# Kernel optimization log

Hardware: AMD Instinct MI355X
Metric: run time of the kernel (lower is better)

Reference implementation:

```python
import jax, jax.numpy as jnp
import numpy as np

B, S, T, D, H, HD = 1, 2048, 256, 3072, 24, 128
FF = 4 * D
EPS_LN = 1e-6
EPS_RMS = 1e-6


def _layernorm(x):
    m = jnp.mean(x, axis=-1, keepdims=True)
    v = jnp.mean(jnp.square(x - m), axis=-1, keepdims=True)
    return (x - m) * jax.lax.rsqrt(v + EPS_LN)


def _rmsnorm(x, w):
    return x * jax.lax.rsqrt(jnp.mean(jnp.square(x), axis=-1, keepdims=True) + EPS_RMS) * w


def _rope_interleaved(x, cos, sin):
    # x: [B,S,H,HD], cos/sin: [S,HD//2]; non-neox (interleaved) style
    x1 = x[..., 0::2]
    x2 = x[..., 1::2]
    c = cos[None, :, None, :]
    s = sin[None, :, None, :]
    o1 = x1 * c - x2 * s
    o2 = x2 * c + x1 * s
    return jnp.stack([o1, o2], axis=-1).reshape(x.shape)


def setup_inputs() -> dict:
    key = jax.random.key(0)
    ks = jax.random.split(key, 12)

    def n(k, shape, scale):
        return jax.random.normal(k, shape, dtype=jnp.float32) * scale

    # real RoPE tables
    pos = np.arange(S, dtype=np.float64)
    inv_freq = 1.0 / (10000.0 ** (np.arange(0, HD, 2, dtype=np.float64) / HD))
    ang = np.outer(pos, inv_freq)  # [S, HD//2]

    return {
        "img": n(ks[0], (B, S, D), 1.0),
        "vec": n(ks[1], (B, D), 1.0),
        "cos": jnp.asarray(np.cos(ang), jnp.float32),
        "sin": jnp.asarray(np.sin(ang), jnp.float32),
        "k_txt": n(ks[2], (B, T, H, HD), 1.0),
        "v_txt": n(ks[3], (B, T, H, HD), 1.0),
        "mod_w": n(ks[4], (D, 6 * D), 0.02),
        "mod_b": jnp.zeros((6 * D,), jnp.float32),
        "qkv_w": n(ks[5], (D, 3 * D), 0.02),
        "qkv_b": jnp.zeros((3 * D,), jnp.float32),
        "qn_w": jnp.ones((HD,), jnp.float32),
        "kn_w": jnp.ones((HD,), jnp.float32),
        "proj_w": n(ks[6], (D, D), 0.02),
        "proj_b": jnp.zeros((D,), jnp.float32),
        "mlp_w1": n(ks[7], (D, FF), 0.02),
        "mlp_b1": jnp.zeros((FF,), jnp.float32),
        "mlp_w2": n(ks[8], (FF, D), 0.02),
        "mlp_b2": jnp.zeros((D,), jnp.float32),
    }


def reference(img, vec, cos, sin, k_txt, v_txt, mod_w, mod_b, qkv_w, qkv_b,
              qn_w, kn_w, proj_w, proj_b, mlp_w1, mlp_b1, mlp_w2, mlp_b2):
    # modulation: silu(vec) -> linear -> 6 chunks, each [B,1,D]
    mod = jax.nn.silu(vec) @ mod_w + mod_b
    (a_shift, a_scale, a_gate, m_shift, m_scale, m_gate) = [
        m[:, None, :] for m in jnp.split(mod, 6, axis=-1)
    ]

    # LayerNorm (no affine) + scale/shift modulate
    x = _layernorm(img) * (1.0 + a_scale) + a_shift

    qkv = (x @ qkv_w + qkv_b).reshape(B, S, 3, H, HD)
    q, k, v = qkv[:, :, 0], qkv[:, :, 1], qkv[:, :, 2]
    q = _rmsnorm(q, qn_w)
    k = _rmsnorm(k, kn_w)
    q = _rope_interleaved(q, cos, sin)
    k = _rope_interleaved(k, cos, sin)

    # concat text KV cache (no RoPE on text tokens)
    k_all = jnp.concatenate([k, k_txt], axis=1)  # [B,S+T,H,HD]
    v_all = jnp.concatenate([v, v_txt], axis=1)

    scale = 1.0 / jnp.sqrt(jnp.asarray(HD, jnp.float32))
    scores = jnp.einsum('bqhd,bkhd->bhqk', q, k_all) * scale
    probs = jax.nn.softmax(scores, axis=-1)
    attn = jnp.einsum('bhqk,bkhd->bqhd', probs, v_all).reshape(B, S, D)

    attn_out = attn @ proj_w + proj_b

    # ScaleResidualLayerNormScaleShift
    residual = img + a_gate * attn_out
    mlp_in = _layernorm(residual) * (1.0 + m_scale) + m_shift

    mlp_out = jax.nn.gelu(mlp_in @ mlp_w1 + mlp_b1, approximate=True) @ mlp_w2 + mlp_b2
    return residual + m_gate * mlp_out
```

## Files before the change

kernel.cpp:

```cpp
#include <hip/hip_runtime.h>

typedef short short8 __attribute__((ext_vector_type(8)));
typedef float f32x4 __attribute__((ext_vector_type(4)));

#define DEV static __device__ __forceinline__

DEV unsigned short f2bf(float f) {
  union { float f; unsigned u; } v; v.f = f;
  unsigned u = v.u;
  unsigned r = u + 0x7fffu + ((u >> 16) & 1u);
  return (unsigned short)(r >> 16);
}
DEV float bf2f(unsigned short b) {
  union { unsigned u; float f; } v; v.u = ((unsigned)b) << 16;
  return v.f;
}
DEV void load_lds16(const void* g, void* l) {
  __builtin_amdgcn_global_load_lds(
      (const __attribute__((address_space(1))) unsigned int*)g,
      (__attribute__((address_space(3))) unsigned int*)l, 16, 0, 0);
}
DEV int swz(int L) { return L ^ ((L >> 3) & 0x30); }

__global__ __launch_bounds__(256) void zero_mod(const float* __restrict__ b, float* __restrict__ out) {
  int j = blockIdx.x * 256 + threadIdx.x;
  out[j] = b[j];
}

__global__ __launch_bounds__(256) void mod_gemv(const float* __restrict__ vec,
                                                const float* __restrict__ W,
                                                float* __restrict__ out) {
  __shared__ float sv[192];
  int tid = threadIdx.x;
  int kb = blockIdx.y * 192;
  if (tid < 192) {
    float x = vec[kb + tid];
    sv[tid] = x / (1.f + __expf(-x));
  }
  __syncthreads();
  int j = blockIdx.x * 256 + tid;
  float a0 = 0, a1 = 0, a2 = 0, a3 = 0;
  for (int i = 0; i < 192; i += 4) {
    a0 += sv[i + 0] * W[(size_t)(kb + i + 0) * 18432 + j];
    a1 += sv[i + 1] * W[(size_t)(kb + i + 1) * 18432 + j];
    a2 += sv[i + 2] * W[(size_t)(kb + i + 2) * 18432 + j];
    a3 += sv[i + 3] * W[(size_t)(kb + i + 3) * 18432 + j];
  }
  atomicAdd(&out[j], a0 + a1 + a2 + a3);
}

__global__ __launch_bounds__(256) void ln_kernel(const float* __restrict__ in,
                                                 const float* __restrict__ mod,
                                                 int shift_off, int scale_off,
                                                 unsigned short* __restrict__ out) {
  int rowb = blockIdx.x;
  const float* x = in + (size_t)rowb * 3072;
  int tid = threadIdx.x;
  float s = 0.f, ss = 0.f;
  float4 v[3];
#pragma unroll
  for (int r = 0; r < 3; r++) {
    v[r] = *(const float4*)&x[r * 1024 + tid * 4];
    s += v[r].x + v[r].y + v[r].z + v[r].w;
    ss += v[r].x * v[r].x + v[r].y * v[r].y + v[r].z * v[r].z + v[r].w * v[r].w;
  }
#pragma unroll
  for (int m = 32; m; m >>= 1) { s += __shfl_xor(s, m); ss += __shfl_xor(ss, m); }
  __shared__ float red[8];
  int w = tid >> 6, lane = tid & 63;
  if (lane == 0) { red[w] = s; red[4 + w] = ss; }
  __syncthreads();
  s = red[0] + red[1] + red[2] + red[3];
  ss = red[4] + red[5] + red[6] + red[7];
  float mean = s * (1.f / 3072.f);
  float var = ss * (1.f / 3072.f) - mean * mean;
  float rstd = rsqrtf(var + 1e-6f);
#pragma unroll
  for (int r = 0; r < 3; r++) {
    int c = r * 1024 + tid * 4;
    float xv[4] = {v[r].x, v[r].y, v[r].z, v[r].w};
#pragma unroll
    for (int i = 0; i < 4; i++) {
      float o = (xv[i] - mean) * rstd * (1.f + mod[scale_off + c + i]) + mod[shift_off + c + i];
      out[(size_t)rowb * 3072 + c + i] = f2bf(o);
    }
  }
}

__global__ __launch_bounds__(256) void transpose_k(const float* __restrict__ src,
                                                   unsigned short* __restrict__ dst,
                                                   int K, int N) {
  __shared__ float t[64][65];
  int n0 = blockIdx.x * 64, k0 = blockIdx.y * 64;
  int tid = threadIdx.x;
#pragma unroll
  for (int i = 0; i < 16; i++) {
    int lin = i * 256 + tid;
    int r = lin >> 6, c = lin & 63;
    t[r][c] = src[(size_t)(k0 + r) * N + n0 + c];
  }
  __syncthreads();
#pragma unroll
  for (int i = 0; i < 16; i++) {
    int lin = i * 256 + tid;
    int rn = lin >> 6, cn = lin & 63;
    dst[(size_t)(n0 + rn) * K + k0 + cn] = f2bf(t[cn][rn]);
  }
}

template <int EPI>
__global__ __launch_bounds__(512, 2) void gemm8(const unsigned short* __restrict__ A,
                                                const unsigned short* __restrict__ Bt,
                                                const float* __restrict__ bias,
                                                unsigned short* __restrict__ outb,
                                                int N, int ldk, int klen) {
  __shared__ unsigned short As[4][8192];
  __shared__ unsigned short Bs[4][8192];
  const int tid = threadIdx.x, lane = tid & 63, w = tid >> 6;
  const int wr = w >> 2, wc = w & 3;
  const int lr = lane & 15, lk = lane >> 4;

  const int bm = blockIdx.y * 256, bn = blockIdx.x * 256;
  const int kbase = blockIdx.z * klen;
  const int NT = klen >> 5;

  const int D0 = tid * 16;
  const int D1 = 8192 + tid * 16;
  const int L0 = swz(D0), L1 = swz(D1);
  const unsigned short* sA0 = A + (size_t)(bm + (L0 >> 6)) * ldk + kbase + ((L0 & 63) >> 1);
  const unsigned short* sA1 = A + (size_t)(bm + (L1 >> 6)) * ldk + kbase + ((L1 & 63) >> 1);
  const unsigned short* sB0 = Bt + (size_t)(bn + (L0 >> 6)) * ldk + kbase + ((L0 & 63) >> 1);
  const unsigned short* sB1 = Bt + (size_t)(bn + (L1 >> 6)) * ldk + kbase + ((L1 & 63) >> 1);

  int aoff[8], boff[4];
#pragma unroll
  for (int mi = 0; mi < 8; mi++)
    aoff[mi] = swz(((wr * 128 + mi * 16 + lr) << 6) | (lk << 4));
#pragma unroll
  for (int ni = 0; ni < 4; ni++)
    boff[ni] = swz(((wc * 64 + ni * 16 + lr) << 6) | (lk << 4));

  f32x4 acc[8][4];
#pragma unroll
  for (int i = 0; i < 8; i++)
#pragma unroll
    for (int j = 0; j < 4; j++) acc[i][j] = (f32x4){0.f, 0.f, 0.f, 0.f};

#pragma unroll
  for (int j = 0; j < 3; j++) {
    load_lds16(sA0 + j * 32, (char*)As + j * 16384 + D0);
    load_lds16(sA1 + j * 32, (char*)As + j * 16384 + D1);
    load_lds16(sB0 + j * 32, (char*)Bs + j * 16384 + D0);
    load_lds16(sB1 + j * 32, (char*)Bs + j * 16384 + D1);
  }
  asm volatile("s_waitcnt vmcnt(8)" ::: "memory");
  __builtin_amdgcn_sched_barrier(0);
  __builtin_amdgcn_s_barrier();

  for (int t = 0; t < NT; ++t) {
    const int rt = t & 3;
    char* Ab = (char*)As + rt * 16384;
    char* Bb = (char*)Bs + rt * 16384;
    const int ss = (t + 3) & 3;
    const int sk = (t + 3) * 32;
    const bool stg = (t + 3) < NT;

    short8 af[8], bf[4];
#pragma unroll
    for (int mi = 0; mi < 8; mi++) af[mi] = *(const short8*)(Ab + aoff[mi]);
#pragma unroll
    for (int ni = 0; ni < 4; ni++) bf[ni] = *(const short8*)(Bb + boff[ni]);
    if (stg) {
      load_lds16(sA0 + sk, (char*)As + ss * 16384 + D0);
      load_lds16(sA1 + sk, (char*)As + ss * 16384 + D1);
      load_lds16(sB0 + sk, (char*)Bs + ss * 16384 + D0);
      load_lds16(sB1 + sk, (char*)Bs + ss * 16384 + D1);
    }
    __builtin_amdgcn_s_setprio(1);
#pragma unroll
    for (int mi = 0; mi < 8; mi++)
#pragma unroll
      for (int ni = 0; ni < 4; ni++)
        acc[mi][ni] = __builtin_amdgcn_mfma_f32_16x16x32_bf16(af[mi], bf[ni], acc[mi][ni], 0, 0, 0);
    __builtin_amdgcn_s_setprio(0);
    if (t < NT - 3) {
      asm volatile("s_waitcnt vmcnt(8)" ::: "memory");
    } else if (t == NT - 3) {
      asm volatile("s_waitcnt vmcnt(4)" ::: "memory");
    } else if (t == NT - 2) {
      asm volatile("s_waitcnt vmcnt(0)" ::: "memory");
    }
    __builtin_amdgcn_sched_barrier(0);
    __builtin_amdgcn_s_barrier();
  }

  const size_t zoff = (size_t)blockIdx.z * ((size_t)2048 * N);
#pragma unroll
  for (int mi = 0; mi < 8; mi++) {
#pragma unroll
    for (int ni = 0; ni < 4; ni++) {
      int row0 = bm + wr * 128 + mi * 16 + lk * 4;
      int col = bn + wc * 64 + ni * 16 + lr;
#pragma unroll
      for (int r = 0; r < 4; r++) {
        float vv = acc[mi][ni][r];
        if (EPI == 0) {
          outb[(size_t)(row0 + r) * N + col] = f2bf(vv + bias[col]);
        } else if (EPI == 2) {
          float x = vv + bias[col];
          float y = 0.7978845608028654f * (x + 0.044715f * x * x * x);
          float th = 1.f - 2.f / (__expf(2.f * y) + 1.f);
          outb[(size_t)(row0 + r) * N + col] = f2bf(0.5f * x * (1.f + th));
        } else {
          outb[zoff + (size_t)(row0 + r) * N + col] = f2bf(vv);
        }
      }
    }
  }
}

__global__ __launch_bounds__(256) void sk_epi(const unsigned short* __restrict__ pb,
                                              const float* __restrict__ bias,
                                              const float* __restrict__ addsrc,
                                              const float* __restrict__ gate,
                                              float* __restrict__ out) {
  const int N = 3072;
  const size_t MN = (size_t)2048 * 3072;
  int row = blockIdx.y;
  int col = blockIdx.x * 1024 + threadIdx.x * 4;
  size_t idx = (size_t)row * N + col;
  const unsigned short* p0 = pb + idx;
  const unsigned short* p1 = pb + MN + idx;
  float4 a = *(const float4*)(addsrc + idx);
  float4 b = *(const float4*)(bias + col);
  float4 g = *(const float4*)(gate + col);
  float4 o;
  o.x = a.x + g.x * (bf2f(p0[0]) + bf2f(p1[0]) + b.x);
  o.y = a.y + g.y * (bf2f(p0[1]) + bf2f(p1[1]) + b.y);
  o.z = a.z + g.z * (bf2f(p0[2]) + bf2f(p1[2]) + b.z);
  o.w = a.w + g.w * (bf2f(p0[3]) + bf2f(p1[3]) + b.w);
  *(float4*)(out + idx) = o;
}

__global__ __launch_bounds__(64) void qkv_post(const unsigned short* __restrict__ qkv,
                                               const float* __restrict__ k_txt,
                                               const float* __restrict__ v_txt,
                                               const float* __restrict__ cosb,
                                               const float* __restrict__ sinb,
                                               const float* __restrict__ qn,
                                               const float* __restrict__ kn,
                                               unsigned short* __restrict__ qb,
                                               unsigned short* __restrict__ kb,
                                               unsigned short* __restrict__ vb) {
  int s = blockIdx.x, h = blockIdx.y;
  int lane = threadIdx.x;
  int d0 = lane * 2;
  if (s < 2048) {
    const unsigned short* rowp = qkv + (size_t)s * 9216;
    float c = cosb[s * 64 + lane], sn = sinb[s * 64 + lane];
    const float ascale = 0.08838834764831845f;
    {
      float a = bf2f(rowp[h * 128 + d0]), b = bf2f(rowp[h * 128 + d0 + 1]);
      float sq = a * a + b * b;
#pragma unroll
      for (int m = 32; m; m >>= 1) sq += __shfl_xor(sq, m);
      float rr = rsqrtf(sq * (1.f / 128.f) + 1e-6f);
      float x1 = a * rr * qn[d0], x2 = b * rr * qn[d0 + 1];
      float o1 = (x1 * c - x2 * sn) * ascale;
      float o2 = (x2 * c + x1 * sn) * ascale;
      size_t off = ((size_t)h * 2048 + s) * 128 + d0;
      qb[off] = f2bf(o1); qb[off + 1] = f2bf(o2);
    }
    {
      float a = bf2f(rowp[3072 + h * 128 + d0]), b = bf2f(rowp[3072 + h * 128 + d0 + 1]);
      float sq = a * a + b * b;
#pragma unroll
      for (int m = 32; m; m >>= 1) sq += __shfl_xor(sq, m);
      float rr = rsqrtf(sq * (1.f / 128.f) + 1e-6f);
      float x1 = a * rr * kn[d0], x2 = b * rr * kn[d0 + 1];
      float o1 = x1 * c - x2 * sn;
      float o2 = x2 * c + x1 * sn;
      size_t off = ((size_t)h * 2304 + s) * 128 + d0;
      kb[off] = f2bf(o1); kb[off + 1] = f2bf(o2);
    }
    {
      float a = bf2f(rowp[6144 + h * 128 + d0]), b = bf2f(rowp[6144 + h * 128 + d0 + 1]);
      size_t off = ((size_t)h * 2304 + s) * 128 + d0;
      vb[off] = f2bf(a); vb[off + 1] = f2bf(b);
    }
  } else {
    int t = s - 2048;
    size_t src = ((size_t)t * 24 + h) * 128 + d0;
    size_t off = ((size_t)h * 2304 + s) * 128 + d0;
    kb[off] = f2bf(k_txt[src]); kb[off + 1] = f2bf(k_txt[src + 1]);
    vb[off] = f2bf(v_txt[src]); vb[off + 1] = f2bf(v_txt[src + 1]);
  }
}

__global__ __launch_bounds__(256) void attn_k(const unsigned short* __restrict__ qb,
                                              const unsigned short* __restrict__ kb,
                                              const unsigned short* __restrict__ vb,
                                              unsigned short* __restrict__ out) {
  __shared__ unsigned short Ks[64 * 128];
  __shared__ unsigned short Vs[128 * 64];
  __shared__ unsigned short Ps[4][16 * 64];
  int h = blockIdx.y, q0 = blockIdx.x * 64;
  int tid = threadIdx.x, lane = tid & 63, w = tid >> 6;
  int lr = lane & 15, lk = lane >> 4;

  const unsigned short* kh = kb + (size_t)h * 2304 * 128;
  const unsigned short* vh = vb + (size_t)h * 2304 * 128;

  short8 qf[4];
#pragma unroll
  for (int kf = 0; kf < 4; kf++)
    qf[kf] = *(const short8*)&qb[((size_t)h * 2048 + q0 + w * 16 + lr) * 128 + kf * 32 + lk * 8];

  float mrow[4] = {-1e30f, -1e30f, -1e30f, -1e30f};
  float lsum[4] = {0.f, 0.f, 0.f, 0.f};
  f32x4 oacc[8];
#pragma unroll
  for (int i = 0; i < 8; i++) oacc[i] = (f32x4){0.f, 0.f, 0.f, 0.f};

  for (int kt = 0; kt < 36; kt++) {
    int kv0 = kt * 64;
    __syncthreads();
#pragma unroll
    for (int i = 0; i < 4; i++) {
      int o = (w * 4 + i) * 1024 + lane * 16;
      int n = o >> 8;
      int sl = (o >> 4) & 15;
      int c = sl ^ (n & 15);
      load_lds16((const char*)(kh + (size_t)(kv0 + n) * 128) + c * 16, (char*)Ks + o);
    }
#pragma unroll
    for (int r = 0; r < 4; r++) {
      int e = r * 2048 + tid * 8;
      int kv = e >> 7, dd0 = e & 127;
      short8 val = *(const short8*)&vh[(size_t)(kv0 + kv) * 128 + dd0];
#pragma unroll
      for (int j = 0; j < 8; j++) {
        int d = dd0 + j;
        int fs = (d & 7) ^ ((d >> 3) & 7);
        Vs[d * 64 + (((kv >> 3) ^ fs) << 3) + (kv & 7)] = (unsigned short)val[j];
      }
    }
    __syncthreads();

    f32x4 sa[4];
#pragma unroll
    for (int ni = 0; ni < 4; ni++) sa[ni] = (f32x4){0.f, 0.f, 0.f, 0.f};
#pragma unroll
    for (int kf = 0; kf < 4; kf++) {
#pragma unroll
      for (int ni = 0; ni < 4; ni++) {
        int n = ni * 16 + lr;
        int slot = (kf * 4 + lk) ^ (n & 15);
        short8 bfr = *(const short8*)&Ks[n * 128 + slot * 8];
        sa[ni] = __builtin_amdgcn_mfma_f32_16x16x32_bf16(qf[kf], bfr, sa[ni], 0, 0, 0);
      }
    }

    float pv[4][4];
#pragma unroll
    for (int r = 0; r < 4; r++) {
      float mx = fmaxf(fmaxf(sa[0][r], sa[1][r]), fmaxf(sa[2][r], sa[3][r]));
#pragma unroll
      for (int m = 8; m; m >>= 1) mx = fmaxf(mx, __shfl_xor(mx, m));
      float mnew = fmaxf(mrow[r], mx);
      float su = 0.f;
#pragma unroll
      for (int ni = 0; ni < 4; ni++) {
        float p = __expf(sa[ni][r] - mnew);
        pv[ni][r] = p;
        su += p;
      }
#pragma unroll
      for (int m = 8; m; m >>= 1) su += __shfl_xor(su, m);
      float alpha = __expf(mrow[r] - mnew);
      lsum[r] = lsum[r] * alpha + su;
      mrow[r] = mnew;
#pragma unroll
      for (int df = 0; df < 8; df++) oacc[df][r] *= alpha;
    }
#pragma unroll
    for (int ni = 0; ni < 4; ni++)
#pragma unroll
      for (int r = 0; r < 4; r++) {
        int row = lk * 4 + r, col = ni * 16 + lr;
        Ps[w][row * 64 + ((((col >> 3) ^ (row & 7))) << 3) + (col & 7)] = f2bf(pv[ni][r]);
      }

#pragma unroll
    for (int kf2 = 0; kf2 < 2; kf2++) {
      short8 pa = *(const short8*)&Ps[w][lr * 64 + (((kf2 * 4 + lk) ^ (lr & 7)) << 3)];
#pragma unroll
      for (int df = 0; df < 8; df++) {
        int d = df * 16 + lr;
        int fs = (d & 7) ^ ((d >> 3) & 7);
        short8 bv = *(const short8*)&Vs[d * 64 + (((kf2 * 4 + lk) ^ fs) << 3)];
        oacc[df] = __builtin_amdgcn_mfma_f32_16x16x32_bf16(pa, bv, oacc[df], 0, 0, 0);
      }
    }
  }

#pragma unroll
  for (int r = 0; r < 4; r++) {
    float inv = 1.f / lsum[r];
    int row = q0 + w * 16 + lk * 4 + r;
#pragma unroll
    for (int df = 0; df < 8; df++)
      out[(size_t)row * 3072 + h * 128 + df * 16 + lr] = f2bf(oacc[df][r] * inv);
  }
}

extern "C" void kernel_launch(void* const* d_in, const int* in_sizes, int n_in,
                              void* d_out, int out_size, void* d_ws, size_t ws_size,
                              hipStream_t stream) {
  const float* img = (const float*)d_in[0];
  const float* vec = (const float*)d_in[1];
  const float* cosb = (const float*)d_in[2];
  const float* sinb = (const float*)d_in[3];
  const float* k_txt = (const float*)d_in[4];
  const float* v_txt = (const float*)d_in[5];
  const float* mod_w = (const float*)d_in[6];
  const float* mod_b = (const float*)d_in[7];
  const float* qkv_w = (const float*)d_in[8];
  const float* qkv_b = (const float*)d_in[9];
  const float* qn_w = (const float*)d_in[10];
  const float* kn_w = (const float*)d_in[11];
  const float* proj_w = (const float*)d_in[12];
  const float* proj_b = (const float*)d_in[13];
  const float* mlp_w1 = (const float*)d_in[14];
  const float* mlp_b1 = (const float*)d_in[15];
  const float* mlp_w2 = (const float*)d_in[16];
  const float* mlp_b2 = (const float*)d_in[17];
  float* outp = (float*)d_out;

  char* ws = (char*)d_ws;
  unsigned short* qkvb = (unsigned short*)(ws + 0);
  unsigned short* qbuf = (unsigned short*)(ws + 37748736);
  unsigned short* kbuf = (unsigned short*)(ws + 50331648);
  unsigned short* vbuf = (unsigned short*)(ws + 64487424);
  unsigned short* attnb = (unsigned short*)(ws + 78643200);
  float* resid = (float*)(ws + 91226112);
  unsigned short* xln = (unsigned short*)(ws + 116391936);
  float* modv = (float*)(ws + 128974848);
  unsigned short* wt = (unsigned short*)(ws + 129048576);
  unsigned short* hbuf = (unsigned short*)(ws + 0);
  unsigned short* pbuf = (unsigned short*)(ws + 50331648);

  zero_mod<<<72, 256, 0, stream>>>(mod_b, modv);
  mod_gemv<<<dim3(72, 16), 256, 0, stream>>>(vec, mod_w, modv);

  ln_kernel<<<2048, 256, 0, stream>>>(img, modv, 0, 3072, xln);

  transpose_k<<<dim3(144, 48), 256, 0, stream>>>(qkv_w, wt, 3072, 9216);
  gemm8<0><<<dim3(36, 8, 1), 512, 0, stream>>>(xln, wt, qkv_b, qkvb, 9216, 3072, 3072);

  qkv_post<<<dim3(2304, 24), 64, 0, stream>>>(qkvb, k_txt, v_txt, cosb, sinb,
                                              qn_w, kn_w, qbuf, kbuf, vbuf);

  attn_k<<<dim3(32, 24), 256, 0, stream>>>(qbuf, kbuf, vbuf, attnb);

  transpose_k<<<dim3(48, 48), 256, 0, stream>>>(proj_w, wt, 3072, 3072);
  gemm8<3><<<dim3(12, 8, 2), 512, 0, stream>>>(attnb, wt, nullptr, pbuf, 3072, 3072, 1536);
  sk_epi<<<dim3(3, 2048), 256, 0, stream>>>(pbuf, proj_b, img, modv + 2 * 3072, resid);

  ln_kernel<<<2048, 256, 0, stream>>>(resid, modv, 3 * 3072, 4 * 3072, xln);

  transpose_k<<<dim3(192, 48), 256, 0, stream>>>(mlp_w1, wt, 3072, 12288);
  gemm8<2><<<dim3(48, 8, 1), 512, 0, stream>>>(xln, wt, mlp_b1, hbuf, 12288, 3072, 3072);

  transpose_k<<<dim3(48, 192), 256, 0, stream>>>(mlp_w2, wt, 12288, 3072);
  gemm8<3><<<dim3(12, 8, 2), 512, 0, stream>>>(hbuf, wt, nullptr, pbuf, 3072, 12288, 6144);
  sk_epi<<<dim3(3, 2048), 256, 0, stream>>>(pbuf, mlp_b2, resid, modv + 5 * 3072, outp);
}
```

Measured before the change: 989.2 us.

## Pre-transpose V and double-buffer K/V tiles in larger attention blocks

```diff
diff --git a/kernel.cpp b/kernel.cpp
--- a/kernel.cpp
+++ b/kernel.cpp
@@ -106,6 +106,26 @@
     int rn = lin >> 6, cn = lin & 63;
     dst[(size_t)(n0 + rn) * K + k0 + cn] = f2bf(t[cn][rn]);
   }
+}
+
+__global__ __launch_bounds__(256) void vt_k(const unsigned short* __restrict__ qkvb,
+                                            const float* __restrict__ v_txt,
+                                            unsigned short* __restrict__ vt) {
+  int h = blockIdx.y;
+  int c8 = blockIdx.x * 2 + (threadIdx.x >> 7);
+  int d = threadIdx.x & 127;
+  int kvb = c8 * 8;
+  short8 o;
+  if (kvb < 2048) {
+#pragma unroll
+    for (int j = 0; j < 8; j++)
+      o[j] = (short)qkvb[(size_t)(kvb + j) * 9216 + 6144 + h * 128 + d];
+  } else {
+#pragma unroll
+    for (int j = 0; j < 8; j++)
+      o[j] = (short)f2bf(v_txt[((size_t)(kvb + j - 2048) * 24 + h) * 128 + d]);
+  }
+  *(short8*)&vt[((size_t)h * 128 + d) * 2304 + kvb] = o;
 }
 
 template <int EPI>
@@ -244,14 +264,12 @@
 
 __global__ __launch_bounds__(64) void qkv_post(const unsigned short* __restrict__ qkv,
                                                const float* __restrict__ k_txt,
-                                               const float* __restrict__ v_txt,
                                                const float* __restrict__ cosb,
                                                const float* __restrict__ sinb,
                                                const float* __restrict__ qn,
                                                const float* __restrict__ kn,
                                                unsigned short* __restrict__ qb,
-                                               unsigned short* __restrict__ kb,
-                                               unsigned short* __restrict__ vb) {
+                                               unsigned short* __restrict__ kb) {
   int s = blockIdx.x, h = blockIdx.y;
   int lane = threadIdx.x;
   int d0 = lane * 2;
@@ -283,134 +301,149 @@
       size_t off = ((size_t)h * 2304 + s) * 128 + d0;
       kb[off] = f2bf(o1); kb[off + 1] = f2bf(o2);
     }
-    {
-      float a = bf2f(rowp[6144 + h * 128 + d0]), b = bf2f(rowp[6144 + h * 128 + d0 + 1]);
-      size_t off = ((size_t)h * 2304 + s) * 128 + d0;
-      vb[off] = f2bf(a); vb[off + 1] = f2bf(b);
-    }
   } else {
     int t = s - 2048;
     size_t src = ((size_t)t * 24 + h) * 128 + d0;
     size_t off = ((size_t)h * 2304 + s) * 128 + d0;
     kb[off] = f2bf(k_txt[src]); kb[off + 1] = f2bf(k_txt[src + 1]);
-    vb[off] = f2bf(v_txt[src]); vb[off + 1] = f2bf(v_txt[src + 1]);
-  }
-}
-
-__global__ __launch_bounds__(256) void attn_k(const unsigned short* __restrict__ qb,
+  }
+}
+
+__global__ __launch_bounds__(512) void attn_k(const unsigned short* __restrict__ qb,
                                               const unsigned short* __restrict__ kb,
-                                              const unsigned short* __restrict__ vb,
+                                              const unsigned short* __restrict__ vt,
                                               unsigned short* __restrict__ out) {
-  __shared__ unsigned short Ks[64 * 128];
-  __shared__ unsigned short Vs[128 * 64];
-  __shared__ unsigned short Ps[4][16 * 64];
-  int h = blockIdx.y, q0 = blockIdx.x * 64;
+  __shared__ unsigned short Ks[2][8192];
+  __shared__ unsigned short Vs[2][8192];
+  __shared__ unsigned short Ps[8][32 * 72];
+  int h = blockIdx.y, q0 = blockIdx.x * 256;
   int tid = threadIdx.x, lane = tid & 63, w = tid >> 6;
   int lr = lane & 15, lk = lane >> 4;
 
   const unsigned short* kh = kb + (size_t)h * 2304 * 128;
-  const unsigned short* vh = vb + (size_t)h * 2304 * 128;
-
-  short8 qf[4];
-#pragma unroll
-  for (int kf = 0; kf < 4; kf++)
-    qf[kf] = *(const short8*)&qb[((size_t)h * 2048 + q0 + w * 16 + lr) * 128 + kf * 32 + lk * 8];
-
-  float mrow[4] = {-1e30f, -1e30f, -1e30f, -1e30f};
-  float lsum[4] = {0.f, 0.f, 0.f, 0.f};
-  f32x4 oacc[8];
-#pragma unroll
-  for (int i = 0; i < 8; i++) oacc[i] = (f32x4){0.f, 0.f, 0.f, 0.f};
+  const unsigned short* vth = vt + (size_t)h * 128 * 2304;
+
+  short8 qf[2][4];
+#pragma unroll
+  for (int mi = 0; mi < 2; mi++)
+#pragma unroll
+    for (int kf = 0; kf < 4; kf++)
+      qf[mi][kf] = *(const short8*)&qb[((size_t)h * 2048 + q0 + w * 32 + mi * 16 + lr) * 128 + kf * 32 + lk * 8];
+
+  const int kR0 = (tid * 16) >> 8, kR1 = (tid * 16 + 8192) >> 8;
+  const int kCc = ((tid * 16) >> 4) & 15;
+  const int kOf0 = kR0 * 128 + ((kCc ^ (kR0 & 15)) * 8);
+  const int kOf1 = kR1 * 128 + ((kCc ^ (kR1 & 15)) * 8);
+  const int vR0 = (tid * 16) >> 7, vR1 = (tid * 16 + 8192) >> 7;
+  const int vCc = ((tid * 16) >> 4) & 7;
+  const int vOf0 = vR0 * 2304 + ((vCc ^ (vR0 & 7)) * 8);
+  const int vOf1 = vR1 * 2304 + ((vCc ^ (vR1 & 7)) * 8);
+
+  float mrow[2][4], lsum[2][4];
+#pragma unroll
+  for (int mi = 0; mi < 2; mi++)
+#pragma unroll
+    for (int r = 0; r < 4; r++) { mrow[mi][r] = -1e30f; lsum[mi][r] = 0.f; }
+  f32x4 oacc[2][8];
+#pragma unroll
+  for (int mi = 0; mi < 2; mi++)
+#pragma unroll
+    for (int i = 0; i < 8; i++) oacc[mi][i] = (f32x4){0.f, 0.f, 0.f, 0.f};
+
+  load_lds16(kh + kOf0, (char*)Ks[0] + tid * 16);
+  load_lds16(kh + kOf1, (char*)Ks[0] + tid * 16 + 8192);
+  load_lds16(vth + vOf0, (char*)Vs[0] + tid * 16);
+  load_lds16(vth + vOf1, (char*)Vs[0] + tid * 16 + 8192);
+  asm volatile("s_waitcnt vmcnt(0)" ::: "memory");
+  __builtin_amdgcn_sched_barrier(0);
+  __builtin_amdgcn_s_barrier();
 
   for (int kt = 0; kt < 36; kt++) {
-    int kv0 = kt * 64;
-    __syncthreads();
-#pragma unroll
-    for (int i = 0; i < 4; i++) {
-      int o = (w * 4 + i) * 1024 + lane * 16;
-      int n = o >> 8;
-      int sl = (o >> 4) & 15;
-      int c = sl ^ (n & 15);
-      load_lds16((const char*)(kh + (size_t)(kv0 + n) * 128) + c * 16, (char*)Ks + o);
-    }
-#pragma unroll
-    for (int r = 0; r < 4; r++) {
-      int e = r * 2048 + tid * 8;
-      int kv = e >> 7, dd0 = e & 127;
-      short8 val = *(const short8*)&vh[(size_t)(kv0 + kv) * 128 + dd0];
-#pragma unroll
-      for (int j = 0; j < 8; j++) {
-        int d = dd0 + j;
-        int fs = (d & 7) ^ ((d >> 3) & 7);
-        Vs[d * 64 + (((kv >> 3) ^ fs) << 3) + (kv & 7)] = (unsigned short)val[j];
-      }
-    }
-    __syncthreads();
-
-    f32x4 sa[4];
-#pragma unroll
-    for (int ni = 0; ni < 4; ni++) sa[ni] = (f32x4){0.f, 0.f, 0.f, 0.f};
+    const int cur = kt & 1, nxt = cur ^ 1;
+    if (kt + 1 < 36) {
+      int kv1 = (kt + 1) * 64;
+      load_lds16(kh + (size_t)kv1 * 128 + kOf0, (char*)Ks[nxt] + tid * 16);
+      load_lds16(kh + (size_t)kv1 * 128 + kOf1, (char*)Ks[nxt] + tid * 16 + 8192);
+      load_lds16(vth + kv1 + vOf0, (char*)Vs[nxt] + tid * 16);
+      load_lds16(vth + kv1 + vOf1, (char*)Vs[nxt] + tid * 16 + 8192);
+    }
+
+    f32x4 sa[2][4];
+#pragma unroll
+    for (int mi = 0; mi < 2; mi++)
+#pragma unroll
+      for (int ni = 0; ni < 4; ni++) sa[mi][ni] = (f32x4){0.f, 0.f, 0.f, 0.f};
+    __builtin_amdgcn_s_setprio(1);
 #pragma unroll
     for (int kf = 0; kf < 4; kf++) {
 #pragma unroll
       for (int ni = 0; ni < 4; ni++) {
         int n = ni * 16 + lr;
-        int slot = (kf * 4 + lk) ^ (n & 15);
-        short8 bfr = *(const short8*)&Ks[n * 128 + slot * 8];
-        sa[ni] = __builtin_amdgcn_mfma_f32_16x16x32_bf16(qf[kf], bfr, sa[ni], 0, 0, 0);
+        short8 bfr = *(const short8*)&Ks[cur][n * 128 + (((kf * 4 + lk) ^ lr) & 15) * 8];
+        sa[0][ni] = __builtin_amdgcn_mfma_f32_16x16x32_bf16(qf[0][kf], bfr, sa[0][ni], 0, 0, 0);
+        sa[1][ni] = __builtin_amdgcn_mfma_f32_16x16x32_bf16(qf[1][kf], bfr, sa[1][ni], 0, 0, 0);
       }
     }
-
-    float pv[4][4];
-#pragma unroll
-    for (int r = 0; r < 4; r++) {
-      float mx = fmaxf(fmaxf(sa[0][r], sa[1][r]), fmaxf(sa[2][r], sa[3][r]));
-#pragma unroll
-      for (int m = 8; m; m >>= 1) mx = fmaxf(mx, __shfl_xor(mx, m));
-      float mnew = fmaxf(mrow[r], mx);
-      float su = 0.f;
-#pragma unroll
-      for (int ni = 0; ni < 4; ni++) {
-        float p = __expf(sa[ni][r] - mnew);
-        pv[ni][r] = p;
-        su += p;
+    __builtin_amdgcn_s_setprio(0);
+
+#pragma unroll
+    for (int mi = 0; mi < 2; mi++) {
+#pragma unroll
+      for (int r = 0; r < 4; r++) {
+        float mx = fmaxf(fmaxf(sa[mi][0][r], sa[mi][1][r]), fmaxf(sa[mi][2][r], sa[mi][3][r]));
+#pragma unroll
+        for (int m = 8; m; m >>= 1) mx = fmaxf(mx, __shfl_xor(mx, m));
+        float mnew = fmaxf(mrow[mi][r], mx);
+        float p0 = __expf(sa[mi][0][r] - mnew);
+        float p1 = __expf(sa[mi][1][r] - mnew);
+        float p2 = __expf(sa[mi][2][r] - mnew);
+        float p3 = __expf(sa[mi][3][r] - mnew);
+        float su = p0 + p1 + p2 + p3;
+#pragma unroll
+        for (int m = 8; m; m >>= 1) su += __shfl_xor(su, m);
+        float alpha = __expf(mrow[mi][r] - mnew);
+        lsum[mi][r] = lsum[mi][r] * alpha + su;
+        mrow[mi][r] = mnew;
+#pragma unroll
+        for (int df = 0; df < 8; df++) oacc[mi][df][r] *= alpha;
+        int prow = (mi * 16 + lk * 4 + r) * 72;
+        Ps[w][prow + 0 * 16 + lr] = f2bf(p0);
+        Ps[w][prow + 1 * 16 + lr] = f2bf(p1);
+        Ps[w][prow + 2 * 16 + lr] = f2bf(p2);
+        Ps[w][prow + 3 * 16 + lr] = f2bf(p3);
       }
-#pragma unroll
-      for (int m = 8; m; m >>= 1) su += __shfl_xor(su, m);
-      float alpha = __expf(mrow[r] - mnew);
-      lsum[r] = lsum[r] * alpha + su;
-      mrow[r] = mnew;
-#pragma unroll
-      for (int df = 0; df < 8; df++) oacc[df][r] *= alpha;
-    }
-#pragma unroll
-    for (int ni = 0; ni < 4; ni++)
-#pragma unroll
-      for (int r = 0; r < 4; r++) {
-        int row = lk * 4 + r, col = ni * 16 + lr;
-        Ps[w][row * 64 + ((((col >> 3) ^ (row & 7))) << 3) + (col & 7)] = f2bf(pv[ni][r]);
-      }
-
+    }
+
+    __builtin_amdgcn_s_setprio(1);
 #pragma unroll
     for (int kf2 = 0; kf2 < 2; kf2++) {
-      short8 pa = *(const short8*)&Ps[w][lr * 64 + (((kf2 * 4 + lk) ^ (lr & 7)) << 3)];
+      short8 pa0 = *(const short8*)&Ps[w][(0 * 16 + lr) * 72 + kf2 * 32 + lk * 8];
+      short8 pa1 = *(const short8*)&Ps[w][(1 * 16 + lr) * 72 + kf2 * 32 + lk * 8];
 #pragma unroll
       for (int df = 0; df < 8; df++) {
         int d = df * 16 + lr;
-        int fs = (d & 7) ^ ((d >> 3) & 7);
-        short8 bv = *(const short8*)&Vs[d * 64 + (((kf2 * 4 + lk) ^ fs) << 3)];
-        oacc[df] = __builtin_amdgcn_mfma_f32_16x16x32_bf16(pa, bv, oacc[df], 0, 0, 0);
+        short8 bv = *(const short8*)&Vs[cur][d * 64 + (((kf2 * 4 + lk) ^ (lr & 7)) & 7) * 8];
+        oacc[0][df] = __builtin_amdgcn_mfma_f32_16x16x32_bf16(pa0, bv, oacc[0][df], 0, 0, 0);
+        oacc[1][df] = __builtin_amdgcn_mfma_f32_16x16x32_bf16(pa1, bv, oacc[1][df], 0, 0, 0);
       }
     }
-  }
-
-#pragma unroll
-  for (int r = 0; r < 4; r++) {
-    float inv = 1.f / lsum[r];
-    int row = q0 + w * 16 + lk * 4 + r;
-#pragma unroll
-    for (int df = 0; df < 8; df++)
-      out[(size_t)row * 3072 + h * 128 + df * 16 + lr] = f2bf(oacc[df][r] * inv);
+    __builtin_amdgcn_s_setprio(0);
+
+    asm volatile("s_waitcnt vmcnt(0)" ::: "memory");
+    __builtin_amdgcn_sched_barrier(0);
+    __builtin_amdgcn_s_barrier();
+  }
+
+#pragma unroll
+  for (int mi = 0; mi < 2; mi++) {
+#pragma unroll
+    for (int r = 0; r < 4; r++) {
+      float inv = 1.f / lsum[mi][r];
+      int row = q0 + w * 32 + mi * 16 + lk * 4 + r;
+#pragma unroll
+      for (int df = 0; df < 8; df++)
+        out[(size_t)row * 3072 + h * 128 + df * 16 + lr] = f2bf(oacc[mi][df][r] * inv);
+    }
   }
 }
 
@@ -441,7 +474,7 @@
   unsigned short* qkvb = (unsigned short*)(ws + 0);
   unsigned short* qbuf = (unsigned short*)(ws + 37748736);
   unsigned short* kbuf = (unsigned short*)(ws + 50331648);
-  unsigned short* vbuf = (unsigned short*)(ws + 64487424);
+  unsigned short* vtbuf = (unsigned short*)(ws + 64487424);
   unsigned short* attnb = (unsigned short*)(ws + 78643200);
   float* resid = (float*)(ws + 91226112);
   unsigned short* xln = (unsigned short*)(ws + 116391936);
@@ -458,10 +491,10 @@
   transpose_k<<<dim3(144, 48), 256, 0, stream>>>(qkv_w, wt, 3072, 9216);
   gemm8<0><<<dim3(36, 8, 1), 512, 0, stream>>>(xln, wt, qkv_b, qkvb, 9216, 3072, 3072);
 
-  qkv_post<<<dim3(2304, 24), 64, 0, stream>>>(qkvb, k_txt, v_txt, cosb, sinb,
-                                              qn_w, kn_w, qbuf, kbuf, vbuf);
-
-  attn_k<<<dim3(32, 24), 256, 0, stream>>>(qbuf, kbuf, vbuf, attnb);
+  qkv_post<<<dim3(2304, 24), 64, 0, stream>>>(qkvb, k_txt, cosb, sinb, qn_w, kn_w, qbuf, kbuf);
+  vt_k<<<dim3(144, 24), 256, 0, stream>>>(qkvb, v_txt, vtbuf);
+
+  attn_k<<<dim3(8, 24), 512, 0, stream>>>(qbuf, kbuf, vtbuf, attnb);
 
   transpose_k<<<dim3(48, 48), 256, 0, stream>>>(proj_w, wt, 3072, 3072);
   gemm8<3><<<dim3(12, 8, 2), 512, 0, stream>>>(attnb, wt, nullptr, pbuf, 3072, 3072, 1536);
```

Result: faster. 958.2 us (-3.1%).
